# Optimization experiments

Measured on AMD Instinct MI355X. Metric: run time of the kernel, lower is better.

## Reference

```python
import jax, jax.numpy as jnp
import numpy as np

N_NODES = 100000
N_EDGES = 3200000
IN_DIM = 256
HID_DIM = 64


def setup_inputs() -> dict:
    key = jax.random.key(0)
    k1, k2, k3 = jax.random.split(key, 3)
    x = jax.random.normal(k1, (N_NODES, IN_DIM), dtype=jnp.float32)
    edge_index = jax.random.randint(k2, (2, N_EDGES), 0, N_NODES, dtype=jnp.int32)
    # Glorot-ish init for the GCN weight
    W = jax.random.normal(k3, (IN_DIM, HID_DIM), dtype=jnp.float32) * (1.0 / np.sqrt(IN_DIM))
    b = jnp.zeros((HID_DIM,), dtype=jnp.float32)
    return {"x": x, "edge_index": edge_index, "W": W, "b": b}


def reference(x, edge_index, W, b):
    N = x.shape[0]
    # --- gcn_norm: add self loops, symmetric degree normalization ---
    loop = jnp.arange(N, dtype=edge_index.dtype)
    row = jnp.concatenate([edge_index[0], loop])  # source nodes
    col = jnp.concatenate([edge_index[1], loop])  # destination nodes
    deg = jax.ops.segment_sum(jnp.ones(row.shape[0], dtype=x.dtype), col, num_segments=N)
    dinv = jnp.where(deg > 0, jax.lax.rsqrt(deg), 0.0)
    norm = dinv[row] * dinv[col]  # [E+N]
    # --- linear transform first (in_dim > out_dim), then aggregate ---
    xt = x @ W  # [N, hid]
    msg = xt[row] * norm[:, None]  # [E+N, hid] gathered messages
    out = jax.ops.segment_sum(msg, col, num_segments=N) + b
    return jax.nn.relu(out)
```

## Files before the change

### kernel.cpp

```cpp
#include <hip/hip_runtime.h>

#define IN_DIM 256
#define HID 64
#define SBSH 8
#define SBN 256
#define NSB_MAX 512

static __device__ __forceinline__ unsigned bf16r(float f) {
    unsigned x = __float_as_uint(f);
    return (x + 0x7fffu + ((x >> 16) & 1u)) >> 16;
}

__global__ void __launch_bounds__(256) k_zero(int* __restrict__ p, int n) {
    int i = blockIdx.x * 256 + threadIdx.x;
    if (i < n) p[i] = 0;
}

__global__ void __launch_bounds__(256) k_chist(const int* __restrict__ col,
                                               int* __restrict__ bucketCnt, int E, int nsb) {
    __shared__ int hist[NSB_MAX];
    const int tid = threadIdx.x;
    const int chunkE = (E + gridDim.x - 1) / gridDim.x;
    const int s = blockIdx.x * chunkE;
    const int e = min(s + chunkE, E);
    for (int i = tid; i < nsb; i += 256) hist[i] = 0;
    __syncthreads();
    for (int j = s + tid; j < e; j += 256) atomicAdd(&hist[col[j] >> SBSH], 1);
    __syncthreads();
    for (int i = tid; i < nsb; i += 256) {
        int h = hist[i];
        if (h) atomicAdd(&bucketCnt[i], h);
    }
}

__global__ void __launch_bounds__(256) k_scanB(const int* __restrict__ bucketCnt,
                                               int* __restrict__ bucketOff,
                                               int* __restrict__ cursorB,
                                               int* __restrict__ rowptr,
                                               int nsb, int N, int E) {
    __shared__ int tmp[256];
    const int tid = threadIdx.x;
    const int PT = (nsb + 255) >> 8;
    int v[8];
    int s = 0;
    for (int k = 0; k < PT; ++k) {
        int i = tid * PT + k;
        v[k] = (i < nsb) ? bucketCnt[i] : 0;
        s += v[k];
    }
    tmp[tid] = s;
    __syncthreads();
    for (int d = 1; d < 256; d <<= 1) {
        int val = (tid >= d) ? tmp[tid - d] : 0;
        __syncthreads();
        tmp[tid] += val;
        __syncthreads();
    }
    int run = tmp[tid] - s;
    for (int k = 0; k < PT; ++k) {
        int i = tid * PT + k;
        if (i < nsb) { bucketOff[i] = run; cursorB[i] = run; }
        run += v[k];
    }
    if (tid == 255) { bucketOff[nsb] = E; rowptr[N] = E; }
}

__global__ void __launch_bounds__(256) k_part2(const int* __restrict__ row,
                                               const int* __restrict__ col,
                                               int* __restrict__ cursorB,
                                               int* __restrict__ part, int E, int nsb) {
    __shared__ int hist[NSB_MAX];
    __shared__ int lcur[NSB_MAX];
    const int tid = threadIdx.x;
    const int chunkE = (E + gridDim.x - 1) / gridDim.x;
    const int s = blockIdx.x * chunkE;
    const int e = min(s + chunkE, E);

    for (int i = tid; i < nsb; i += 256) hist[i] = 0;
    __syncthreads();
    for (int j = s + tid; j < e; j += 256) atomicAdd(&hist[col[j] >> SBSH], 1);
    __syncthreads();
    for (int i = tid; i < nsb; i += 256) {
        int h = hist[i];
        lcur[i] = h ? atomicAdd(&cursorB[i], h) : 0;
    }
    __syncthreads();
    for (int j = s + tid; j < e; j += 256) {
        int c = col[j];
        int pos = atomicAdd(&lcur[c >> SBSH], 1);
        part[pos] = (row[j] << SBSH) | (c & (SBN - 1));
    }
}

__global__ void __launch_bounds__(256) k_sortb(const int* __restrict__ bucketOff,
                                               const int* __restrict__ part,
                                               int* __restrict__ rowptr,
                                               float* __restrict__ dinv,
                                               int* __restrict__ eRow, int N) {
    __shared__ int hcnt[SBN];
    __shared__ int tmp[SBN];
    __shared__ int cur[SBN];
    const int tid = threadIdx.x;
    const int base = blockIdx.x << SBSH;
    const int s = bucketOff[blockIdx.x];
    const int e = bucketOff[blockIdx.x + 1];

    hcnt[tid] = 0;
    __syncthreads();
    for (int j = s + tid; j < e; j += 256) atomicAdd(&hcnt[part[j] & (SBN - 1)], 1);
    __syncthreads();
    const int c = hcnt[tid];
    tmp[tid] = c;
    __syncthreads();
    for (int d = 1; d < 256; d <<= 1) {
        int val = (tid >= d) ? tmp[tid - d] : 0;
        __syncthreads();
        tmp[tid] += val;
        __syncthreads();
    }
    const int myBase = s + tmp[tid] - c;
    cur[tid] = myBase;
    const int n = base + tid;
    if (n < N) {
        rowptr[n] = myBase;
        dinv[n] = __frsqrt_rn((float)(c + 1));
    }
    __syncthreads();
    for (int j = s + tid; j < e; j += 256) {
        int p = part[j];
        int pos = atomicAdd(&cur[p & (SBN - 1)], 1);
        eRow[pos] = p >> SBSH;
    }
}

__global__ void __launch_bounds__(256) k_gemm(const float* __restrict__ x,
                                              const float* __restrict__ W,
                                              const float* __restrict__ dinv,
                                              unsigned* __restrict__ xsb, int N) {
    __shared__ float xT[32][260];
    __shared__ float Wl[32][64];
    const int t = threadIdx.x;
    const int tmI = t >> 3;
    const int tnI = t & 7;
    const int nodeBase = blockIdx.x * 256;

    float acc[8][8] = {};

    for (int k0 = 0; k0 < IN_DIM; k0 += 32) {
#pragma unroll
        for (int i = 0; i < 2; ++i) {
            int flat = i * 256 + t;
            float4 wv = ((const float4*)W)[k0 * 16 + flat];
            *(float4*)&Wl[flat >> 4][(flat & 15) << 2] = wv;
        }
#pragma unroll
        for (int i = 0; i < 8; ++i) {
            int flat = i * 256 + t;
            int n = flat >> 3;
            int kq = (flat & 7) << 2;
            int gn = nodeBase + n;
            if (gn >= N) gn = N - 1;
            float4 v = *(const float4*)(x + (size_t)gn * IN_DIM + k0 + kq);
            xT[kq + 0][n] = v.x;
            xT[kq + 1][n] = v.y;
            xT[kq + 2][n] = v.z;
            xT[kq + 3][n] = v.w;
        }
        __syncthreads();
#pragma unroll
        for (int k = 0; k < 32; ++k) {
            float xv[8], wv[8];
            *(float4*)&xv[0] = *(const float4*)&xT[k][tmI * 8];
            *(float4*)&xv[4] = *(const float4*)&xT[k][tmI * 8 + 4];
            *(float4*)&wv[0] = *(const float4*)&Wl[k][tnI * 8];
            *(float4*)&wv[4] = *(const float4*)&Wl[k][tnI * 8 + 4];
#pragma unroll
            for (int mi = 0; mi < 8; ++mi)
#pragma unroll
                for (int ni = 0; ni < 8; ++ni)
                    acc[mi][ni] = fmaf(xv[mi], wv[ni], acc[mi][ni]);
        }
        __syncthreads();
    }

#pragma unroll
    for (int mi = 0; mi < 8; ++mi) {
        int n = nodeBase + tmI * 8 + mi;
        if (n < N) {
            float d = dinv[n];
            uint4 o;
            o.x = bf16r(acc[mi][0] * d) | (bf16r(acc[mi][1] * d) << 16);
            o.y = bf16r(acc[mi][2] * d) | (bf16r(acc[mi][3] * d) << 16);
            o.z = bf16r(acc[mi][4] * d) | (bf16r(acc[mi][5] * d) << 16);
            o.w = bf16r(acc[mi][6] * d) | (bf16r(acc[mi][7] * d) << 16);
            *(uint4*)(xsb + (size_t)n * (HID / 2) + tnI * 4) = o;
        }
    }
}

__global__ void __launch_bounds__(256) k_agg(const int* __restrict__ rowptr,
                                             const int* __restrict__ eRow,
                                             const unsigned* __restrict__ xsb,
                                             const float* __restrict__ dinv,
                                             const float* __restrict__ bias,
                                             float* __restrict__ out, int N) {
    const int lane = threadIdx.x & 63;
    const int l = lane & 31;
    const int n = (blockIdx.x * 4 + (threadIdx.x >> 6)) * 2 + (lane >> 5);
    if (n >= N) return;

    const int s = rowptr[n];
    const int e = rowptr[n + 1];

    unsigned u = xsb[(size_t)n * 32 + l];
    float ax = __uint_as_float(u << 16), ay = __uint_as_float(u & 0xffff0000u);
    float b0x = 0.f, b0y = 0.f, b1x = 0.f, b1y = 0.f;
    float b2x = 0.f, b2y = 0.f, b3x = 0.f, b3y = 0.f;
    int j = s;
    for (; j + 3 < e; j += 4) {
        unsigned u0 = xsb[(size_t)eRow[j] * 32 + l];
        unsigned u1 = xsb[(size_t)eRow[j + 1] * 32 + l];
        unsigned u2 = xsb[(size_t)eRow[j + 2] * 32 + l];
        unsigned u3 = xsb[(size_t)eRow[j + 3] * 32 + l];
        b0x += __uint_as_float(u0 << 16); b0y += __uint_as_float(u0 & 0xffff0000u);
        b1x += __uint_as_float(u1 << 16); b1y += __uint_as_float(u1 & 0xffff0000u);
        b2x += __uint_as_float(u2 << 16); b2y += __uint_as_float(u2 & 0xffff0000u);
        b3x += __uint_as_float(u3 << 16); b3y += __uint_as_float(u3 & 0xffff0000u);
    }
    for (; j < e; ++j) {
        unsigned u0 = xsb[(size_t)eRow[j] * 32 + l];
        ax += __uint_as_float(u0 << 16); ay += __uint_as_float(u0 & 0xffff0000u);
    }
    ax += (b0x + b1x) + (b2x + b3x);
    ay += (b0y + b1y) + (b2y + b3y);

    const float d = dinv[n];
    const float2 bl = *(const float2*)&bias[2 * l];
    float2 o;
    o.x = fmaxf(fmaf(ax, d, bl.x), 0.f);
    o.y = fmaxf(fmaf(ay, d, bl.y), 0.f);
    *(float2*)(out + (size_t)n * HID + 2 * l) = o;
}

extern "C" void kernel_launch(void* const* d_in, const int* in_sizes, int n_in,
                              void* d_out, int out_size, void* d_ws, size_t ws_size,
                              hipStream_t stream) {
    const float* x  = (const float*)d_in[0];
    const int*   ei = (const int*)d_in[1];
    const float* W  = (const float*)d_in[2];
    const float* b  = (const float*)d_in[3];
    float* out = (float*)d_out;

    const int N = in_sizes[0] / IN_DIM;
    const int E = in_sizes[1] / 2;
    const int* row = ei;
    const int* col = ei + E;
    const int NSB = (N + SBN - 1) >> SBSH;

    int*      bucketCnt = (int*)d_ws;
    int*      bucketOff = bucketCnt + NSB;
    int*      cursorB   = bucketOff + NSB + 1;
    int*      rowptr    = cursorB + NSB;
    float*    dinv      = (float*)(rowptr + N + 1);
    unsigned* xsb       = (unsigned*)(dinv + N);
    int*      part      = (int*)(xsb + (size_t)N * (HID / 2));
    int*      eRow      = part + E;

    k_zero<<<(NSB + 255) / 256, 256, 0, stream>>>(bucketCnt, NSB);
    k_chist<<<256, 256, 0, stream>>>(col, bucketCnt, E, NSB);
    k_scanB<<<1, 256, 0, stream>>>(bucketCnt, bucketOff, cursorB, rowptr, NSB, N, E);
    k_part2<<<256, 256, 0, stream>>>(row, col, cursorB, part, E, NSB);
    k_sortb<<<NSB, 256, 0, stream>>>(bucketOff, part, rowptr, dinv, eRow, N);
    k_gemm<<<(N + 255) / 256, 256, 0, stream>>>(x, W, dinv, xsb, N);
    k_agg<<<(N + 7) / 8, 256, 0, stream>>>(rowptr, eRow, xsb, dinv, b, out, N);
}
```

Baseline: 415.1 us.

## Store per-block bucket histograms to skip re-counting in partition pass

The partition stage now keeps each block's bucket histogram in a global table, scans it per bucket in a new kernel to get deterministic per-block cursors, and the scatter kernel loads those cursors instead of rebuilding the histogram and taking global atomics. This removes a second full read of col and the atomic cursor allocation, at the cost of an extra launch and a small histogram table in workspace. Separately, the aggregation loop is unrolled to 8 edges so more gathers are in flight at once.

```diff
diff --git a/kernel.cpp b/kernel.cpp
--- a/kernel.cpp
+++ b/kernel.cpp
@@ -5,37 +5,41 @@
 #define SBSH 8
 #define SBN 256
 #define NSB_MAX 512
+#define PB 256
 
 static __device__ __forceinline__ unsigned bf16r(float f) {
     unsigned x = __float_as_uint(f);
     return (x + 0x7fffu + ((x >> 16) & 1u)) >> 16;
 }
 
+static __device__ __forceinline__ float blo(unsigned u) { return __uint_as_float(u << 16); }
+static __device__ __forceinline__ float bhi(unsigned u) { return __uint_as_float(u & 0xffff0000u); }
+
 __global__ void __launch_bounds__(256) k_zero(int* __restrict__ p, int n) {
     int i = blockIdx.x * 256 + threadIdx.x;
     if (i < n) p[i] = 0;
 }
 
-__global__ void __launch_bounds__(256) k_chist(const int* __restrict__ col,
-                                               int* __restrict__ bucketCnt, int E, int nsb) {
+__global__ void __launch_bounds__(256) k_p2a(const int* __restrict__ col,
+                                             int* __restrict__ bucketCnt,
+                                             int* __restrict__ blkHist, int E, int nsb) {
     __shared__ int hist[NSB_MAX];
-    const int tid = threadIdx.x;
-    const int chunkE = (E + gridDim.x - 1) / gridDim.x;
-    const int s = blockIdx.x * chunkE;
-    const int e = min(s + chunkE, E);
+    const int tid = threadIdx.x, b = blockIdx.x;
+    const int chunkE = (E + PB - 1) / PB;
+    const int s = b * chunkE, e = min(s + chunkE, E);
     for (int i = tid; i < nsb; i += 256) hist[i] = 0;
     __syncthreads();
     for (int j = s + tid; j < e; j += 256) atomicAdd(&hist[col[j] >> SBSH], 1);
     __syncthreads();
     for (int i = tid; i < nsb; i += 256) {
         int h = hist[i];
+        blkHist[i * PB + b] = h;
         if (h) atomicAdd(&bucketCnt[i], h);
     }
 }
 
 __global__ void __launch_bounds__(256) k_scanB(const int* __restrict__ bucketCnt,
                                                int* __restrict__ bucketOff,
-                                               int* __restrict__ cursorB,
                                                int* __restrict__ rowptr,
                                                int nsb, int N, int E) {
     __shared__ int tmp[256];
@@ -59,31 +63,38 @@
     int run = tmp[tid] - s;
     for (int k = 0; k < PT; ++k) {
         int i = tid * PT + k;
-        if (i < nsb) { bucketOff[i] = run; cursorB[i] = run; }
+        if (i < nsb) bucketOff[i] = run;
         run += v[k];
     }
     if (tid == 255) { bucketOff[nsb] = E; rowptr[N] = E; }
 }
 
-__global__ void __launch_bounds__(256) k_part2(const int* __restrict__ row,
-                                               const int* __restrict__ col,
-                                               int* __restrict__ cursorB,
-                                               int* __restrict__ part, int E, int nsb) {
-    __shared__ int hist[NSB_MAX];
+__global__ void __launch_bounds__(256) k_scanBlk(const int* __restrict__ bucketOff,
+                                                 const int* __restrict__ blkHist,
+                                                 int* __restrict__ blkCur) {
+    __shared__ int tmp[PB];
+    const int i = blockIdx.x, t = threadIdx.x;
+    int v = blkHist[i * PB + t];
+    tmp[t] = v;
+    __syncthreads();
+    for (int d = 1; d < PB; d <<= 1) {
+        int val = (t >= d) ? tmp[t - d] : 0;
+        __syncthreads();
+        tmp[t] += val;
+        __syncthreads();
+    }
+    blkCur[i * PB + t] = bucketOff[i] + tmp[t] - v;
+}
+
+__global__ void __launch_bounds__(256) k_p2b(const int* __restrict__ row,
+                                             const int* __restrict__ col,
+                                             const int* __restrict__ blkCur,
+                                             int* __restrict__ part, int E, int nsb) {
     __shared__ int lcur[NSB_MAX];
-    const int tid = threadIdx.x;
-    const int chunkE = (E + gridDim.x - 1) / gridDim.x;
-    const int s = blockIdx.x * chunkE;
-    const int e = min(s + chunkE, E);
-
-    for (int i = tid; i < nsb; i += 256) hist[i] = 0;
-    __syncthreads();
-    for (int j = s + tid; j < e; j += 256) atomicAdd(&hist[col[j] >> SBSH], 1);
-    __syncthreads();
-    for (int i = tid; i < nsb; i += 256) {
-        int h = hist[i];
-        lcur[i] = h ? atomicAdd(&cursorB[i], h) : 0;
-    }
+    const int tid = threadIdx.x, b = blockIdx.x;
+    const int chunkE = (E + PB - 1) / PB;
+    const int s = b * chunkE, e = min(s + chunkE, E);
+    for (int i = tid; i < nsb; i += 256) lcur[i] = blkCur[i * PB + b];
     __syncthreads();
     for (int j = s + tid; j < e; j += 256) {
         int c = col[j];
@@ -213,23 +224,44 @@
     const int e = rowptr[n + 1];
 
     unsigned u = xsb[(size_t)n * 32 + l];
-    float ax = __uint_as_float(u << 16), ay = __uint_as_float(u & 0xffff0000u);
+    float ax = blo(u), ay = bhi(u);
     float b0x = 0.f, b0y = 0.f, b1x = 0.f, b1y = 0.f;
     float b2x = 0.f, b2y = 0.f, b3x = 0.f, b3y = 0.f;
     int j = s;
+    for (; j + 7 < e; j += 8) {
+        int r0 = eRow[j],     r1 = eRow[j + 1], r2 = eRow[j + 2], r3 = eRow[j + 3];
+        int r4 = eRow[j + 4], r5 = eRow[j + 5], r6 = eRow[j + 6], r7 = eRow[j + 7];
+        unsigned u0 = xsb[(size_t)r0 * 32 + l];
+        unsigned u1 = xsb[(size_t)r1 * 32 + l];
+        unsigned u2 = xsb[(size_t)r2 * 32 + l];
+        unsigned u3 = xsb[(size_t)r3 * 32 + l];
+        unsigned u4 = xsb[(size_t)r4 * 32 + l];
+        unsigned u5 = xsb[(size_t)r5 * 32 + l];
+        unsigned u6 = xsb[(size_t)r6 * 32 + l];
+        unsigned u7 = xsb[(size_t)r7 * 32 + l];
+        b0x += blo(u0); b0y += bhi(u0);
+        b1x += blo(u1); b1y += bhi(u1);
+        b2x += blo(u2); b2y += bhi(u2);
+        b3x += blo(u3); b3y += bhi(u3);
+        b0x += blo(u4); b0y += bhi(u4);
+        b1x += blo(u5); b1y += bhi(u5);
+        b2x += blo(u6); b2y += bhi(u6);
+        b3x += blo(u7); b3y += bhi(u7);
+    }
     for (; j + 3 < e; j += 4) {
-        unsigned u0 = xsb[(size_t)eRow[j] * 32 + l];
-        unsigned u1 = xsb[(size_t)eRow[j + 1] * 32 + l];
-        unsigned u2 = xsb[(size_t)eRow[j + 2] * 32 + l];
-        unsigned u3 = xsb[(size_t)eRow[j + 3] * 32 + l];
-        b0x += __uint_as_float(u0 << 16); b0y += __uint_as_float(u0 & 0xffff0000u);
-        b1x += __uint_as_float(u1 << 16); b1y += __uint_as_float(u1 & 0xffff0000u);
-        b2x += __uint_as_float(u2 << 16); b2y += __uint_as_float(u2 & 0xffff0000u);
-        b3x += __uint_as_float(u3 << 16); b3y += __uint_as_float(u3 & 0xffff0000u);
+        int r0 = eRow[j], r1 = eRow[j + 1], r2 = eRow[j + 2], r3 = eRow[j + 3];
+        unsigned u0 = xsb[(size_t)r0 * 32 + l];
+        unsigned u1 = xsb[(size_t)r1 * 32 + l];
+        unsigned u2 = xsb[(size_t)r2 * 32 + l];
+        unsigned u3 = xsb[(size_t)r3 * 32 + l];
+        b0x += blo(u0); b0y += bhi(u0);
+        b1x += blo(u1); b1y += bhi(u1);
+        b2x += blo(u2); b2y += bhi(u2);
+        b3x += blo(u3); b3y += bhi(u3);
     }
     for (; j < e; ++j) {
         unsigned u0 = xsb[(size_t)eRow[j] * 32 + l];
-        ax += __uint_as_float(u0 << 16); ay += __uint_as_float(u0 & 0xffff0000u);
+        ax += blo(u0); ay += bhi(u0);
     }
     ax += (b0x + b1x) + (b2x + b3x);
     ay += (b0y + b1y) + (b2y + b3y);
@@ -259,17 +291,19 @@
 
     int*      bucketCnt = (int*)d_ws;
     int*      bucketOff = bucketCnt + NSB;
-    int*      cursorB   = bucketOff + NSB + 1;
-    int*      rowptr    = cursorB + NSB;
+    int*      rowptr    = bucketOff + NSB + 1;
     float*    dinv      = (float*)(rowptr + N + 1);
     unsigned* xsb       = (unsigned*)(dinv + N);
     int*      part      = (int*)(xsb + (size_t)N * (HID / 2));
     int*      eRow      = part + E;
+    int*      blkHist   = eRow + E;
+    int*      blkCur    = blkHist + NSB * PB;
 
     k_zero<<<(NSB + 255) / 256, 256, 0, stream>>>(bucketCnt, NSB);
-    k_chist<<<256, 256, 0, stream>>>(col, bucketCnt, E, NSB);
-    k_scanB<<<1, 256, 0, stream>>>(bucketCnt, bucketOff, cursorB, rowptr, NSB, N, E);
-    k_part2<<<256, 256, 0, stream>>>(row, col, cursorB, part, E, NSB);
+    k_p2a<<<PB, 256, 0, stream>>>(col, bucketCnt, blkHist, E, NSB);
+    k_scanB<<<1, 256, 0, stream>>>(bucketCnt, bucketOff, rowptr, NSB, N, E);
+    k_scanBlk<<<NSB, PB, 0, stream>>>(bucketOff, blkHist, blkCur);
+    k_p2b<<<PB, 256, 0, stream>>>(row, col, blkCur, part, E, NSB);
     k_sortb<<<NSB, 256, 0, stream>>>(bucketOff, part, rowptr, dinv, eRow, N);
     k_gemm<<<(N + 255) / 256, 256, 0, stream>>>(x, W, dinv, xsb, N);
     k_agg<<<(N + 7) / 8, 256, 0, stream>>>(rowptr, eRow, xsb, dinv, b, out, N);
```

After: 401.5 us. -3.3%, faster.
